# Performance work log

Measured on AMD Instinct MI355X. Metric: run time of the kernel, lower is better.

## Reference

```python
import jax, jax.numpy as jnp
import numpy as np

HID = 64  # GRU hidden size fixed in source: layers.GRU(64, ...)


def setup_inputs() -> dict:
    key = jax.random.key(0)
    ks = jax.random.split(key, 9)
    B, T, D, K = 128, 1024, 128, 32
    s = 0.05
    X = jax.random.normal(ks[0], (B, T, D), jnp.float32)
    mask = jnp.ones((B, T), jnp.int32)  # 1 = valid token
    # Keras GRU (reset_after=True) params
    gru_kernel = jax.random.normal(ks[1], (D, 3 * HID), jnp.float32) * s
    gru_rec_kernel = jax.random.normal(ks[2], (HID, 3 * HID), jnp.float32) * s
    gru_bias = jax.random.normal(ks[3], (2, 3 * HID), jnp.float32) * s  # [input_bias, recurrent_bias]
    # tfa.layers.CRF params: dense projection + chain kernel + boundary energies
    dense_kernel = jax.random.normal(ks[4], (HID, K), jnp.float32) * s
    dense_bias = jax.random.normal(ks[5], (K,), jnp.float32) * s
    chain_kernel = jax.random.normal(ks[6], (K, K), jnp.float32) * s
    left_boundary = jax.random.normal(ks[7], (K,), jnp.float32) * s
    right_boundary = jax.random.normal(ks[8], (K,), jnp.float32) * s
    return {"X": X, "mask": mask, "gru_kernel": gru_kernel,
            "gru_rec_kernel": gru_rec_kernel, "gru_bias": gru_bias,
            "dense_kernel": dense_kernel, "dense_bias": dense_bias,
            "chain_kernel": chain_kernel, "left_boundary": left_boundary,
            "right_boundary": right_boundary}


def gru_forward(X, mask_bool, gru_kernel, gru_rec_kernel, gru_bias):
    # Keras GRU, reset_after=True: z/r/h gate ordering, tanh/sigmoid activations.
    B, T, D = X.shape
    xproj = X @ gru_kernel + gru_bias[0]  # [B,T,3H] input projection (fused GEMM)

    def step(h, inp):
        xp, mt = inp  # xp: [B,3H], mt: [B] bool
        rec = h @ gru_rec_kernel + gru_bias[1]  # [B,3H]
        xz, xr, xh = jnp.split(xp, 3, axis=-1)
        rz, rr, rh = jnp.split(rec, 3, axis=-1)
        z = jax.nn.sigmoid(xz + rz)
        r = jax.nn.sigmoid(xr + rr)
        hh = jnp.tanh(xh + r * rh)
        hn = z * h + (1.0 - z) * hh
        hn = jnp.where(mt[:, None], hn, h)  # masked steps carry state
        return hn, hn

    h0 = jnp.zeros((B, HID), X.dtype)
    _, hs = jax.lax.scan(step, h0, (jnp.swapaxes(xproj, 0, 1), jnp.swapaxes(mask_bool, 0, 1)))
    return jnp.swapaxes(hs, 0, 1)  # [B,T,H]


def viterbi_decode(potentials, chain_kernel):
    # Max-plus DP with backpointers; potentials: [B,T,K]
    pots = jnp.swapaxes(potentials, 0, 1)  # [T,B,K]

    def fwd(score, pot_t):
        s = score[:, :, None] + chain_kernel[None]  # [B,K_from,K_to]
        bp = jnp.argmax(s, axis=1).astype(jnp.int32)  # [B,K]
        new_score = jnp.max(s, axis=1) + pot_t
        return new_score, bp

    final_score, bps = jax.lax.scan(fwd, pots[0], pots[1:])  # bps: [T-1,B,K]
    last_tag = jnp.argmax(final_score, axis=-1).astype(jnp.int32)  # [B]

    def back(tag, bp):
        prev = jnp.take_along_axis(bp, tag[:, None], axis=1)[:, 0]
        return prev, tag

    first_tag, tags = jax.lax.scan(back, last_tag, bps, reverse=True)  # tags[t] = tag at step t+1
    decoded = jnp.concatenate([first_tag[None], tags], axis=0)  # [T,B]
    return jnp.swapaxes(decoded, 0, 1)  # [B,T]


def reference(X, mask, gru_kernel, gru_rec_kernel, gru_bias,
              dense_kernel, dense_bias, chain_kernel,
              left_boundary, right_boundary):
    B, T, D = X.shape
    mask_bool = mask == 1
    hidden = gru_forward(X, mask_bool, gru_kernel, gru_rec_kernel, gru_bias)
    potentials = hidden @ dense_kernel + dense_bias  # [B,T,K] emissions
    seq_len = jnp.sum(mask, axis=1).astype(jnp.int32)  # [B]
    # Boundary energies (tfa CRF use_boundary=True): left at t=0, right at last valid step
    potentials = potentials.at[:, 0].add(left_boundary)
    potentials = potentials.at[jnp.arange(B), seq_len - 1].add(right_boundary)
    decoded = viterbi_decode(potentials, chain_kernel)  # [B,T] int32
    return decoded, potentials, seq_len, chain_kernel
```

## Files before the change

### kernel.cpp

```cpp
#include <hip/hip_runtime.h>
#include <math.h>

#define BB 128
#define TT 1024
#define DD 128
#define HH 64
#define G3 192
#define KK 32

__global__ __launch_bounds__(256, 2) void xproj_kernel(const float* __restrict__ X,
                                                       const float* __restrict__ Wk,
                                                       const float* __restrict__ gbias,
                                                       float* __restrict__ xp) {
    __shared__ float Xs[64 * 132];
    __shared__ float Ws[128 * 68];
    const int tid = threadIdx.x;
    const int row0 = blockIdx.x * 64;
    const int cg = blockIdx.y;
#pragma unroll
    for (int it = 0; it < 8; ++it) {
        int idx = it * 1024 + tid * 4;
        int r = idx >> 7, c = idx & 127;
        float4 v = *(const float4*)&X[((size_t)(row0 + r)) * DD + c];
        *(float4*)&Xs[r * 132 + c] = v;
    }
#pragma unroll
    for (int it = 0; it < 8; ++it) {
        int idx = it * 1024 + tid * 4;
        int k = idx >> 6, c = idx & 63;
        float4 v = *(const float4*)&Wk[(size_t)k * G3 + cg * 64 + c];
        *(float4*)&Ws[k * 68 + c] = v;
    }
    __syncthreads();
    const int tr = tid >> 4, tc = tid & 15;
    const int r0 = tr * 4, c0 = tc * 4;
    float acc[4][4];
#pragma unroll
    for (int r = 0; r < 4; ++r)
#pragma unroll
        for (int c = 0; c < 4; ++c) acc[r][c] = 0.f;
#pragma unroll 4
    for (int k = 0; k < DD; k += 4) {
        float a[4][4];
#pragma unroll
        for (int r = 0; r < 4; ++r) {
            float4 t = *(const float4*)&Xs[(r0 + r) * 132 + k];
            a[r][0] = t.x; a[r][1] = t.y; a[r][2] = t.z; a[r][3] = t.w;
        }
#pragma unroll
        for (int kk = 0; kk < 4; ++kk) {
            float4 b = *(const float4*)&Ws[(k + kk) * 68 + c0];
#pragma unroll
            for (int r = 0; r < 4; ++r) {
                acc[r][0] += a[r][kk] * b.x;
                acc[r][1] += a[r][kk] * b.y;
                acc[r][2] += a[r][kk] * b.z;
                acc[r][3] += a[r][kk] * b.w;
            }
        }
    }
    float4 bias = *(const float4*)&gbias[cg * 64 + c0];
#pragma unroll
    for (int r = 0; r < 4; ++r) {
        float4 o;
        o.x = acc[r][0] + bias.x; o.y = acc[r][1] + bias.y;
        o.z = acc[r][2] + bias.z; o.w = acc[r][3] + bias.w;
        *(float4*)&xp[((size_t)(row0 + r0 + r)) * G3 + cg * 64 + c0] = o;
    }
}

#define BCAST(v, l) __int_as_float(__builtin_amdgcn_readlane(__float_as_int(v), (l)))

__global__ __launch_bounds__(384, 1)
void fused_kernel(const float* __restrict__ xp,
                  const float* __restrict__ Wr,
                  const float* __restrict__ gbias,
                  const int* __restrict__ mask,
                  const float* __restrict__ Dk,
                  const float* __restrict__ db,
                  const float* __restrict__ chain,
                  const float* __restrict__ lb,
                  const float* __restrict__ rb,
                  float* __restrict__ out_pot,
                  float* __restrict__ out_dec,
                  float* __restrict__ out_slen,
                  float* __restrict__ out_chn) {
    const int b = blockIdx.x;
    const int tid = threadIdx.x;
    const int w = tid >> 6;
    const int l = tid & 63;
    const int bTT = b * TT;

    __shared__ unsigned char bp[(TT - 1) * KK];
    __shared__ unsigned char table[32 * 32 * KK];
    __shared__ int ent[32];
    __shared__ int last_tag_s;
    __shared__ float gbuf[2][4 * HH];
    __shared__ __align__(16) float hbuf[4][HH];
    __shared__ float potbuf[4][KK];

    if (w < 3) {
        const int j = l;
        float wg[HH];
#pragma unroll
        for (int i2 = 0; i2 < HH; ++i2) wg[i2] = Wr[i2 * G3 + w * HH + j];
#pragma unroll
        for (int i2 = 0; i2 < HH; ++i2) asm volatile("" : "+v"(wg[i2]));
        const float bw = gbias[G3 + w * HH + j];
        float h = 0.f;
        const float* xpb = xp + (size_t)bTT * G3;
        float xv0 = xpb[tid];
        float xv1 = xpb[G3 + tid];
        int m0 = mask[bTT];
        int m1 = mask[bTT + 1];
        for (int i = 0; i < TT + 2; ++i) {
            if (i < TT) {
                float a0 = bw, a1 = 0.f, a2 = 0.f, a3 = 0.f;
#pragma unroll
                for (int c = 0; c < HH; c += 4) {
                    a0 += BCAST(h, c + 0) * wg[c + 0];
                    a1 += BCAST(h, c + 1) * wg[c + 1];
                    a2 += BCAST(h, c + 2) * wg[c + 2];
                    a3 += BCAST(h, c + 3) * wg[c + 3];
                }
                float a = (a0 + a1) + (a2 + a3);
                float g = (w == 2) ? a : 1.f / (1.f + __expf(-(xv0 + a)));
                gbuf[i & 1][w * HH + j] = g;
                if (w == 2) gbuf[i & 1][3 * HH + j] = xv0;
            }
            __syncthreads();
            if (i < TT) {
                float z  = gbuf[i & 1][j];
                float r  = gbuf[i & 1][HH + j];
                float rh = gbuf[i & 1][2 * HH + j];
                float xh = gbuf[i & 1][3 * HH + j];
                float y = xh + r * rh;
                float hh = 1.f - 2.f / (1.f + __expf(2.f * y));
                float hn = z * h + (1.f - z) * hh;
                hn = (m0 != 0) ? hn : h;
                h = hn;
                if (w == 0) hbuf[i & 3][j] = hn;
                const int t2 = (i + 2 < TT) ? i + 2 : TT - 1;
                xv0 = xv1; xv1 = xpb[(size_t)t2 * G3 + tid];
                m0 = m1;  m1 = mask[bTT + t2];
            }
        }
    } else if (w == 3) {
        const int k = l & 31;
        int sl = 0;
#pragma unroll
        for (int q = 0; q < 16; ++q) sl += mask[bTT + q * 64 + l];
#pragma unroll
        for (int d = 32; d >= 1; d >>= 1) sl += __shfl_xor(sl, d, 64);
        if (l == 0) out_slen[b] = (float)sl;
        float dk[HH];
#pragma unroll
        for (int i2 = 0; i2 < HH; ++i2) dk[i2] = Dk[i2 * KK + k];
#pragma unroll
        for (int i2 = 0; i2 < HH; ++i2) asm volatile("" : "+v"(dk[i2]));
        const float dbk = db[k], lbk = lb[k], rbk = rb[k];
        float* potb = out_pot + (size_t)bTT * KK;
        for (int i = 0; i < TT + 2; ++i) {
            const int t = i - 2;
            if (t >= 0 && t < TT) {
                const float4* hv4 = (const float4*)&hbuf[t & 3][0];
                float p0 = dbk, p1 = 0.f, p2 = 0.f, p3 = 0.f;
#pragma unroll
                for (int c = 0; c < 16; ++c) {
                    float4 hv = hv4[c];
                    p0 += hv.x * dk[4 * c + 0];
                    p1 += hv.y * dk[4 * c + 1];
                    p2 += hv.z * dk[4 * c + 2];
                    p3 += hv.w * dk[4 * c + 3];
                }
                float pot = (p0 + p1) + (p2 + p3);
                if (t == 0) pot += lbk;
                if (t == sl - 1) pot += rbk;
                if (l < 32) {
                    potbuf[t & 3][k] = pot;
                    potb[(size_t)t * KK + k] = pot;
                }
            }
            __syncthreads();
        }
    } else if (w == 4) {
        const int k = l & 31;
        const int hf = l >> 5;
        float ccol[16];
        int addr[16];
#pragma unroll
        for (int m = 0; m < 16; ++m) {
            ccol[m] = chain[(hf * 16 + m) * KK + k];
            addr[m] = (hf * 16 + m) * 4;
        }
#pragma unroll
        for (int m = 0; m < 16; ++m) asm volatile("" : "+v"(ccol[m]));
        const int addrx = (l ^ 32) * 4;
        float s = 0.f;
        for (int i = 0; i < TT + 2; ++i) {
            __syncthreads();
            const int t = i - 2;
            if (t >= 0 && t < TT) {
                float pot = potbuf[t & 3][k];
                if (t == 0) {
                    s = pot;
                } else {
                    const int si = __float_as_int(s);
                    float c[16];
#pragma unroll
                    for (int m = 0; m < 16; ++m)
                        c[m] = __int_as_float(__builtin_amdgcn_ds_bpermute(addr[m], si)) + ccol[m];
                    float v1[8]; int i1[8];
#pragma unroll
                    for (int p = 0; p < 8; ++p) {
                        bool tk = c[2 * p + 1] > c[2 * p];
                        v1[p] = tk ? c[2 * p + 1] : c[2 * p];
                        i1[p] = hf * 16 + (tk ? 2 * p + 1 : 2 * p);
                    }
                    float v2[4]; int i2[4];
#pragma unroll
                    for (int p = 0; p < 4; ++p) {
                        bool tk = v1[2 * p + 1] > v1[2 * p];
                        v2[p] = tk ? v1[2 * p + 1] : v1[2 * p];
                        i2[p] = tk ? i1[2 * p + 1] : i1[2 * p];
                    }
                    float v3[2]; int i3[2];
#pragma unroll
                    for (int p = 0; p < 2; ++p) {
                        bool tk = v2[2 * p + 1] > v2[2 * p];
                        v3[p] = tk ? v2[2 * p + 1] : v2[2 * p];
                        i3[p] = tk ? i2[2 * p + 1] : i2[2 * p];
                    }
                    bool tk = v3[1] > v3[0];
                    float bv = tk ? v3[1] : v3[0];
                    int bi = tk ? i3[1] : i3[0];
                    float ov = __int_as_float(__builtin_amdgcn_ds_bpermute(addrx, __float_as_int(bv)));
                    int   oi = __builtin_amdgcn_ds_bpermute(addrx, bi);
                    bool take = (ov > bv) || (ov == bv && oi < bi);
                    if (take) { bv = ov; bi = oi; }
                    if (l < 32) bp[(t - 1) * KK + k] = (unsigned char)bi;
                    s = bv + pot;
                }
            }
        }
        float bv = s; int bi = k;
#pragma unroll
        for (int d = 16; d >= 1; d >>= 1) {
            float ov = __shfl_xor(bv, d, 64);
            int   oi = __shfl_xor(bi, d, 64);
            bool take = (ov > bv) || (ov == bv && oi < bi);
            if (take) { bv = ov; bi = oi; }
        }
        if (l == 0) last_tag_s = bi;
    } else {
        for (int i = 0; i < TT + 2; ++i) __syncthreads();
    }
    __syncthreads();
    {
        const int k = tid & 31;
        const int grp = tid >> 5;
        for (int c = grp; c < 32; c += 12) {
            int tag = k;
            for (int ll = 31; ll >= 0; --ll) {
                const int t = c * 32 + ll;
                if (t < TT - 1) tag = bp[t * KK + tag];
                table[(c * 32 + ll) * KK + k] = (unsigned char)tag;
            }
        }
    }
    __syncthreads();
    if (tid == 0) {
        int e = last_tag_s;
        ent[31] = e;
        for (int c = 30; c >= 0; --c) { e = table[(c + 1) * 32 * KK + e]; ent[c] = e; }
    }
    __syncthreads();
    for (int t = tid; t < TT; t += 384) {
        const int c = t >> 5, ll = t & 31;
        out_dec[(size_t)bTT + t] = (float)table[(c * 32 + ll) * KK + ent[c]];
    }
    if (b == 0) {
        for (int i2 = tid; i2 < KK * KK; i2 += 384) out_chn[i2] = chain[i2];
    }
}

extern "C" void kernel_launch(void* const* d_in, const int* in_sizes, int n_in,
                              void* d_out, int out_size, void* d_ws, size_t ws_size,
                              hipStream_t stream) {
    const float* X     = (const float*)d_in[0];
    const int*   mask  = (const int*)d_in[1];
    const float* Wk    = (const float*)d_in[2];
    const float* Wr    = (const float*)d_in[3];
    const float* gb    = (const float*)d_in[4];
    const float* Dk    = (const float*)d_in[5];
    const float* db    = (const float*)d_in[6];
    const float* chain = (const float*)d_in[7];
    const float* lb    = (const float*)d_in[8];
    const float* rb    = (const float*)d_in[9];

    float* out = (float*)d_out;
    float* out_dec  = out;
    float* out_pot  = out + (size_t)BB * TT;
    float* out_slen = out + (size_t)BB * TT + (size_t)BB * TT * KK;
    float* out_chn  = out_slen + BB;

    float* xp = (float*)d_ws;

    xproj_kernel<<<dim3((BB * TT) / 64, 3), dim3(256), 0, stream>>>(X, Wk, gb, xp);
    fused_kernel<<<dim3(BB), dim3(384), 0, stream>>>(xp, Wr, gb, mask, Dk, db, chain,
                                                     lb, rb, out_pot, out_dec,
                                                     out_slen, out_chn);
}
```

Before: 901.2 us.

## Stage xproj and mask chunks in LDS and batch potential stores via ring

The emission wavefront now double-buffers 32-step chunks of the input projection and mask into shared memory, so the recurrent wavefronts read from LDS instead of global memory on the critical serial path. Potentials go into a 64-entry shared ring and are written to global memory in 32-step float4 batches, lagging behind the steps being computed. The idle sixth wavefront is removed (block size drops to 320) and the GRU waves get raised scheduling priority. This adds shared-memory footprint and puts the bulk copy work on the emission wave, which is already on the per-step barrier path.

```diff
diff --git a/kernel.cpp b/kernel.cpp
--- a/kernel.cpp
+++ b/kernel.cpp
@@ -7,6 +7,7 @@
 #define HH 64
 #define G3 192
 #define KK 32
+#define CH 32
 
 __global__ __launch_bounds__(256, 2) void xproj_kernel(const float* __restrict__ X,
                                                        const float* __restrict__ Wk,
@@ -71,7 +72,7 @@
 
 #define BCAST(v, l) __int_as_float(__builtin_amdgcn_readlane(__float_as_int(v), (l)))
 
-__global__ __launch_bounds__(384, 1)
+__global__ __launch_bounds__(320, 1)
 void fused_kernel(const float* __restrict__ xp,
                   const float* __restrict__ Wr,
                   const float* __restrict__ gbias,
@@ -97,7 +98,9 @@
     __shared__ int last_tag_s;
     __shared__ float gbuf[2][4 * HH];
     __shared__ __align__(16) float hbuf[4][HH];
-    __shared__ float potbuf[4][KK];
+    __shared__ __align__(16) float potring[64][KK];
+    __shared__ __align__(16) float xpstage[2][CH * G3];
+    __shared__ int maskst[2][CH];
 
     if (w < 3) {
         const int j = l;
@@ -107,12 +110,11 @@
 #pragma unroll
         for (int i2 = 0; i2 < HH; ++i2) asm volatile("" : "+v"(wg[i2]));
         const float bw = gbias[G3 + w * HH + j];
+        __builtin_amdgcn_s_setprio(1);
         float h = 0.f;
-        const float* xpb = xp + (size_t)bTT * G3;
-        float xv0 = xpb[tid];
-        float xv1 = xpb[G3 + tid];
-        int m0 = mask[bTT];
-        int m1 = mask[bTT + 1];
+        __syncthreads();
+        float xv0 = xpstage[0][tid];
+        int m0 = maskst[0][0];
         for (int i = 0; i < TT + 2; ++i) {
             if (i < TT) {
                 float a0 = bw, a1 = 0.f, a2 = 0.f, a3 = 0.f;
@@ -140,9 +142,11 @@
                 hn = (m0 != 0) ? hn : h;
                 h = hn;
                 if (w == 0) hbuf[i & 3][j] = hn;
-                const int t2 = (i + 2 < TT) ? i + 2 : TT - 1;
-                xv0 = xv1; xv1 = xpb[(size_t)t2 * G3 + tid];
-                m0 = m1;  m1 = mask[bTT + t2];
+                if (i < TT - 1) {
+                    const int t1 = i + 1;
+                    xv0 = xpstage[(t1 >> 5) & 1][(t1 & 31) * G3 + tid];
+                    m0  = maskst[(t1 >> 5) & 1][t1 & 31];
+                }
             }
         }
     } else if (w == 3) {
@@ -159,8 +163,39 @@
 #pragma unroll
         for (int i2 = 0; i2 < HH; ++i2) asm volatile("" : "+v"(dk[i2]));
         const float dbk = db[k], lbk = lb[k], rbk = rb[k];
-        float* potb = out_pot + (size_t)bTT * KK;
+        const float* xpg = xp + (size_t)bTT * G3;
+        float* potg = out_pot + (size_t)bTT * KK;
+#pragma unroll
+        for (int q = 0; q < 24; ++q) {
+            float4 v = *(const float4*)&xpg[q * 256 + l * 4];
+            *(float4*)&xpstage[0][q * 256 + l * 4] = v;
+        }
+        if (l < CH) maskst[0][l] = mask[bTT + l];
+        __syncthreads();
         for (int i = 0; i < TT + 2; ++i) {
+            if ((i & 31) == 0) {
+                const int cn = (i >> 5) + 1;
+                if (cn < 32) {
+                    const float* src = xpg + (size_t)cn * CH * G3;
+                    float* dst = &xpstage[cn & 1][0];
+#pragma unroll
+                    for (int q = 0; q < 24; ++q) {
+                        float4 v = *(const float4*)&src[q * 256 + l * 4];
+                        *(float4*)&dst[q * 256 + l * 4] = v;
+                    }
+                    if (l < CH) maskst[cn & 1][l] = mask[bTT + cn * CH + l];
+                }
+                const int cf = (i >> 5) - 2;
+                if (cf >= 0) {
+                    const float* srcl = &potring[(cf & 1) * 32][0];
+                    float* dstg = potg + (size_t)cf * CH * KK;
+#pragma unroll
+                    for (int q = 0; q < 4; ++q) {
+                        float4 v = *(const float4*)&srcl[q * 256 + l * 4];
+                        *(float4*)&dstg[q * 256 + l * 4] = v;
+                    }
+                }
+            }
             const int t = i - 2;
             if (t >= 0 && t < TT) {
                 const float4* hv4 = (const float4*)&hbuf[t & 3][0];
@@ -176,14 +211,20 @@
                 float pot = (p0 + p1) + (p2 + p3);
                 if (t == 0) pot += lbk;
                 if (t == sl - 1) pot += rbk;
-                if (l < 32) {
-                    potbuf[t & 3][k] = pot;
-                    potb[(size_t)t * KK + k] = pot;
-                }
+                if (l < 32) potring[t & 63][k] = pot;
             }
             __syncthreads();
         }
-    } else if (w == 4) {
+        {
+            const float* srcl = &potring[(31 & 1) * 32][0];
+            float* dstg = potg + (size_t)31 * CH * KK;
+#pragma unroll
+            for (int q = 0; q < 4; ++q) {
+                float4 v = *(const float4*)&srcl[q * 256 + l * 4];
+                *(float4*)&dstg[q * 256 + l * 4] = v;
+            }
+        }
+    } else {
         const int k = l & 31;
         const int hf = l >> 5;
         float ccol[16];
@@ -197,11 +238,12 @@
         for (int m = 0; m < 16; ++m) asm volatile("" : "+v"(ccol[m]));
         const int addrx = (l ^ 32) * 4;
         float s = 0.f;
+        __syncthreads();
         for (int i = 0; i < TT + 2; ++i) {
             __syncthreads();
             const int t = i - 2;
             if (t >= 0 && t < TT) {
-                float pot = potbuf[t & 3][k];
+                float pot = potring[t & 63][k];
                 if (t == 0) {
                     s = pot;
                 } else {
@@ -252,14 +294,12 @@
             if (take) { bv = ov; bi = oi; }
         }
         if (l == 0) last_tag_s = bi;
-    } else {
-        for (int i = 0; i < TT + 2; ++i) __syncthreads();
     }
     __syncthreads();
     {
         const int k = tid & 31;
         const int grp = tid >> 5;
-        for (int c = grp; c < 32; c += 12) {
+        for (int c = grp; c < 32; c += 10) {
             int tag = k;
             for (int ll = 31; ll >= 0; --ll) {
                 const int t = c * 32 + ll;
@@ -275,12 +315,12 @@
         for (int c = 30; c >= 0; --c) { e = table[(c + 1) * 32 * KK + e]; ent[c] = e; }
     }
     __syncthreads();
-    for (int t = tid; t < TT; t += 384) {
+    for (int t = tid; t < TT; t += 320) {
         const int c = t >> 5, ll = t & 31;
         out_dec[(size_t)bTT + t] = (float)table[(c * 32 + ll) * KK + ent[c]];
     }
     if (b == 0) {
-        for (int i2 = tid; i2 < KK * KK; i2 += 384) out_chn[i2] = chain[i2];
+        for (int i2 = tid; i2 < KK * KK; i2 += 320) out_chn[i2] = chain[i2];
     }
 }
 
@@ -307,7 +347,7 @@
     float* xp = (float*)d_ws;
 
     xproj_kernel<<<dim3((BB * TT) / 64, 3), dim3(256), 0, stream>>>(X, Wk, gb, xp);
-    fused_kernel<<<dim3(BB), dim3(384), 0, stream>>>(xp, Wr, gb, mask, Dk, db, chain,
+    fused_kernel<<<dim3(BB), dim3(320), 0, stream>>>(xp, Wr, gb, mask, Dk, db, chain,
                                                      lb, rb, out_pot, out_dec,
                                                      out_slen, out_chn);
 }
```

New measurement: 896.7 us. About the same (-0.5%).
